# Kernel tuning notes

Hardware: AMD Instinct MI355X
Metric: run time of the kernel (lower is better)

Reference implementation:

```python
import jax, jax.numpy as jnp
import numpy as np

IN_DIM = 3072
OUT_DIM = 3072
NUM_GROUPS = 12
RANK = 1024
IN_PG = IN_DIM // NUM_GROUPS    # 256
OUT_PG = OUT_DIM // NUM_GROUPS  # 256


def _xavier_uniform(key, shape):
    # torch xavier_uniform on a 3D tensor treats dim0*..*dim[-2] as fan_in-ish;
    # torch uses fan_in = shape[-1]*prod(shape[1:-1])? Actually for >2D,
    # fan_in = shape[1] * receptive_field, fan_out = shape[0] * receptive_field.
    # For (g, i, r): fan_in = i * r? torch: fan_in = size(1)*rf, fan_out = size(0)*rf
    # where rf = prod(shape[2:]). So fan_in = shape[1]*shape[2], fan_out = shape[0]*shape[2].
    rf = int(np.prod(shape[2:])) if len(shape) > 2 else 1
    fan_in = shape[1] * rf
    fan_out = shape[0] * rf
    limit = float(np.sqrt(6.0 / (fan_in + fan_out)))
    return jax.random.uniform(key, shape, jnp.float32, -limit, limit)


def setup_inputs() -> dict:
    key = jax.random.key(0)
    kx, kd, ku = jax.random.split(key, 3)
    x = jax.random.normal(kx, (2, 4096, IN_DIM), jnp.float32)
    down = _xavier_uniform(kd, (NUM_GROUPS, IN_PG, RANK))
    up = _xavier_uniform(ku, (NUM_GROUPS, RANK, OUT_PG))
    mix = jnp.zeros((NUM_GROUPS, NUM_GROUPS, RANK), jnp.float32)
    idx = jnp.arange(NUM_GROUPS)
    mix = mix.at[idx, idx, :].set(1.0)
    return {"x": x, "down": down, "mix": mix, "up": up}


def reference(x, down, mix, up):
    b, l, _ = x.shape
    xg = x.reshape(b, l, NUM_GROUPS, IN_PG)          # [b,l,g,i]
    z = jnp.einsum('blgi,gir->blgr', xg, down)       # grouped down-project
    z = jnp.einsum('blgr,ghr->blhr', z, mix)         # per-rank group mix (12x12)
    y = jnp.einsum('blhr,hro->blho', z, up)          # grouped up-project
    return y.reshape(b, l, OUT_DIM)
```

## Files before the change

### kernel.cpp

```cpp
#include <hip/hip_runtime.h>
#include <stdint.h>

typedef short  s16x8 __attribute__((ext_vector_type(8)));
typedef short  s16x4 __attribute__((ext_vector_type(4)));
typedef float  f32x4 __attribute__((ext_vector_type(4)));
typedef unsigned short ushort_t;

#define G_AS __attribute__((address_space(1)))
#define L_AS __attribute__((address_space(3)))

__device__ __forceinline__ void gl_lds16(const void* g, void* l) {
    __builtin_amdgcn_global_load_lds((const G_AS uint32_t*)g, (L_AS uint32_t*)l, 16, 0, 0);
}

__device__ __forceinline__ float b2f(ushort_t u) {
    union { uint32_t i; float f; } v; v.i = ((uint32_t)u) << 16; return v.f;
}
__device__ __forceinline__ ushort_t f2b(float f) {
    uint32_t x = __float_as_uint(f);
    x += 0x7FFF + ((x >> 16) & 1);
    return (ushort_t)(x >> 16);
}

#define MFMA16(a, b, c) __builtin_amdgcn_mfma_f32_16x16x32_bf16((a), (b), (c), 0, 0, 0)

__global__ __launch_bounds__(256) void k_cvt(const float* __restrict__ src,
                                             ushort_t* __restrict__ dst, int n8) {
    int idx = blockIdx.x * 256 + threadIdx.x;
    int stride = gridDim.x * 256;
    for (int i = idx; i < n8; i += stride) {
        f32x4 a = *(const f32x4*)(src + (size_t)i * 8);
        f32x4 b = *(const f32x4*)(src + (size_t)i * 8 + 4);
        s16x8 v;
#pragma unroll
        for (int j = 0; j < 4; ++j) { v[j] = (short)f2b(a[j]); v[j + 4] = (short)f2b(b[j]); }
        *(s16x8*)(dst + (size_t)i * 8) = v;
    }
}

__global__ __launch_bounds__(256) void k_transpose_up(const float* __restrict__ up,
                                                      ushort_t* __restrict__ upT) {
    int bid = blockIdx.x;
    int h  = bid >> 6;
    int rt = (bid >> 2) & 15;
    int ot = bid & 3;
    int r0 = rt << 6, o0 = ot << 6;
    __shared__ ushort_t tile[64][72];
    int t = threadIdx.x;
    const float* src = up + ((size_t)h << 18) + (size_t)r0 * 256 + o0;
#pragma unroll
    for (int p = 0; p < 2; ++p) {
        int rr = (t >> 3) + (p << 5);
        int cc = (t & 7) << 3;
        f32x4 va = *(const f32x4*)(src + rr * 256 + cc);
        f32x4 vb = *(const f32x4*)(src + rr * 256 + cc + 4);
#pragma unroll
        for (int j = 0; j < 4; ++j) {
            tile[rr][cc + j]     = f2b(va[j]);
            tile[rr][cc + 4 + j] = f2b(vb[j]);
        }
    }
    __syncthreads();
    ushort_t* dst = upT + ((size_t)h << 18) + (size_t)o0 * 1024 + r0;
#pragma unroll
    for (int p = 0; p < 2; ++p) {
        int oo = (t >> 3) + (p << 5);
        int rr = (t & 7) << 3;
        s16x8 v;
#pragma unroll
        for (int j = 0; j < 8; ++j) v[j] = (short)tile[rr + j][oo];
        *(s16x8*)(dst + (size_t)oo * 1024 + rr) = v;
    }
}

__global__ __launch_bounds__(256) void k_build_w(const ushort_t* __restrict__ downB,
                                                 const float* __restrict__ mixp,
                                                 const ushort_t* __restrict__ upT,
                                                 ushort_t* __restrict__ WT) {
    int bid = blockIdx.x;
    int gh = bid >> 2;
    int g = gh / 12, h = gh % 12;
    int it = (bid >> 1) & 1, ot = bid & 1;
    int i0 = it << 7, o0 = ot << 7;

    const ushort_t* A    = downB + ((size_t)g << 18);
    const ushort_t* Bt   = upT   + ((size_t)h << 18);
    const float*    mrow = mixp  + (size_t)(g * 12 + h) * 1024;

    __shared__ ushort_t As[128 * 64];
    __shared__ ushort_t Bs[128 * 64];

    int tid  = threadIdx.x;
    int lane = tid & 63, wave = tid >> 6;
    int wr = wave >> 1, wc = wave & 1;
    int lr = lane & 15;
    int kq = (lane >> 4) << 3;

    f32x4 acc[4][4] = {};

    for (int kk = 0; kk < 1024; kk += 64) {
        __syncthreads();
#pragma unroll
        for (int j = 0; j < 4; ++j) {
            int off = (j << 12) + (wave << 10) + (lane << 4);
            int row = off >> 7;
            int kc  = (off & 127) >> 1;
            gl_lds16(A  + (size_t)(i0 + row) * 1024 + kk + kc, (char*)As + off);
            gl_lds16(Bt + (size_t)(o0 + row) * 1024 + kk + kc, (char*)Bs + off);
        }
        __syncthreads();
#pragma unroll
        for (int ks = 0; ks < 64; ks += 32) {
            f32x4 m0 = *(const f32x4*)(mrow + kk + ks + kq);
            f32x4 m1 = *(const f32x4*)(mrow + kk + ks + kq + 4);
            float mf[8];
#pragma unroll
            for (int j = 0; j < 4; ++j) { mf[j] = m0[j]; mf[j + 4] = m1[j]; }

            s16x8 bfr[4];
#pragma unroll
            for (int b = 0; b < 4; ++b) {
                s16x8 raw = *(const s16x8*)&Bs[(wc * 64 + b * 16 + lr) * 64 + ks + kq];
#pragma unroll
                for (int j = 0; j < 8; ++j)
                    bfr[b][j] = (short)f2b(b2f((ushort_t)raw[j]) * mf[j]);
            }
            s16x8 afr[4];
#pragma unroll
            for (int a = 0; a < 4; ++a)
                afr[a] = *(const s16x8*)&As[(wr * 64 + a * 16 + lr) * 64 + ks + kq];
#pragma unroll
            for (int a = 0; a < 4; ++a)
#pragma unroll
                for (int b = 0; b < 4; ++b)
                    acc[a][b] = MFMA16(afr[a], bfr[b], acc[a][b]);
        }
    }

    int colbase = g * 256 + i0 + wr * 64;
    int rowbase = h * 256 + o0 + wc * 64;
#pragma unroll
    for (int a = 0; a < 4; ++a)
#pragma unroll
        for (int b = 0; b < 4; ++b) {
            int o = rowbase + b * 16 + lr;
            int i = colbase + a * 16 + ((lane >> 4) << 2);
            s16x4 pv;
#pragma unroll
            for (int v = 0; v < 4; ++v) pv[v] = (short)f2b(acc[a][b][v]);
            *(s16x4*)(WT + (size_t)o * 3072 + i) = pv;
        }
}

#define BAR() __builtin_amdgcn_s_barrier()
#define WAITV(n) asm volatile("s_waitcnt vmcnt(" #n ")" ::: "memory")
#define WAITL() asm volatile("s_waitcnt lgkmcnt(0)" ::: "memory")

__global__ __launch_bounds__(512, 1) void k_main8(const ushort_t* __restrict__ X,
                                                  const ushort_t* __restrict__ WT,
                                                  float* __restrict__ Y) {
    extern __shared__ ushort_t lds[];
    int bid = blockIdx.x;
    int wg  = (bid & 7) * 48 + (bid >> 3);
    int tt = wg / 12, nt = wg % 12;
    int m0 = tt << 8, n0 = nt << 8;

    int tid  = threadIdx.x;
    int lane = tid & 63;
    int wave = tid >> 6;
    int wr = wave >> 2;
    int wc = wave & 3;
    int lr = lane & 15;
    int cq = lane >> 4;

    auto STAGE = [&](int buf, int op, int kh, int t) {
        const ushort_t* src = op ? WT : X;
        int rb = op ? n0 : m0;
        int kb = t * 64 + kh * 32;
        ushort_t* base = lds + buf * 32768 + op * 16384 + kh * 8192;
#pragma unroll
        for (int j = 0; j < 2; ++j) {
            int boff = (j << 13) + (tid << 4);
            int r  = boff >> 6;
            int ch = (boff >> 4) & 3;
            int ks = kb + ((ch ^ ((r >> 1) & 3)) << 3);
            gl_lds16(src + (size_t)(rb + r) * 3072 + ks, (char*)base + boff);
        }
    };
    auto RD = [&](int buf, int op, int kh, int fr) -> s16x8 {
        int row = (op ? wc * 64 : wr * 128) + fr * 16 + lr;
        int off = buf * 32768 + op * 16384 + kh * 8192 + row * 32
                + ((cq ^ ((row >> 1) & 3)) << 3);
        return *(const s16x8*)(lds + off);
    };

    f32x4 acc[8][4] = {};
    s16x8 af[4], bf[4];

#define PH_READ_AB(mlo, kh) { _Pragma("unroll") for (int i = 0; i < 4; ++i) af[i] = RD(cur, 0, kh, (mlo) + i); \
                              _Pragma("unroll") for (int i = 0; i < 4; ++i) bf[i] = RD(cur, 1, kh, i); }
#define PH_READ_A(mlo, kh)  { _Pragma("unroll") for (int i = 0; i < 4; ++i) af[i] = RD(cur, 0, kh, (mlo) + i); }
#define PH_MFMA(mlo)        { __builtin_amdgcn_s_setprio(1); \
                              _Pragma("unroll") for (int mi = 0; mi < 4; ++mi) \
                              _Pragma("unroll") for (int ni = 0; ni < 4; ++ni) \
                                  acc[(mlo) + mi][ni] = MFMA16(af[mi], bf[ni], acc[(mlo) + mi][ni]); \
                              __builtin_amdgcn_s_setprio(0); }

    STAGE(0, 0, 0, 0); STAGE(0, 1, 0, 0); STAGE(0, 0, 1, 0); STAGE(0, 1, 1, 0);
    WAITV(4); BAR();

    int cur = 0;
    for (int t = 0; t < 47; ++t) {
        int nx = cur ^ 1;
        PH_READ_AB(0, 0); STAGE(nx, 0, 0, t + 1);
        BAR(); WAITL(); PH_MFMA(0); BAR();
        PH_READ_A(4, 0);  STAGE(nx, 1, 0, t + 1);
        BAR(); WAITL(); PH_MFMA(4); WAITV(4); BAR();
        PH_READ_AB(0, 1); STAGE(nx, 0, 1, t + 1);
        BAR(); WAITL(); PH_MFMA(0); BAR();
        PH_READ_A(4, 1);  STAGE(nx, 1, 1, t + 1);
        BAR(); WAITL(); PH_MFMA(4); WAITV(4); BAR();
        cur = nx;
    }
    PH_READ_AB(0, 0); BAR(); WAITL(); PH_MFMA(0); BAR();
    PH_READ_A(4, 0);  BAR(); WAITL(); PH_MFMA(4); WAITV(0); BAR();
    PH_READ_AB(0, 1); BAR(); WAITL(); PH_MFMA(0); BAR();
    PH_READ_A(4, 1);  BAR(); WAITL(); PH_MFMA(4);

    int trow = m0 + wr * 128 + (cq << 2);
    int ncol = n0 + wc * 64 + lr;
#pragma unroll
    for (int mi = 0; mi < 8; ++mi)
#pragma unroll
        for (int ni = 0; ni < 4; ++ni) {
            int rr = trow + mi * 16;
            int cc = ncol + ni * 16;
#pragma unroll
            for (int v = 0; v < 4; ++v)
                Y[(size_t)(rr + v) * 3072 + cc] = acc[mi][ni][v];
        }
}

extern "C" void kernel_launch(void* const* d_in, const int* in_sizes, int n_in,
                              void* d_out, int out_size, void* d_ws, size_t ws_size,
                              hipStream_t stream) {
    const float* x    = (const float*)d_in[0];
    const float* down = (const float*)d_in[1];
    const float* mixp = (const float*)d_in[2];
    const float* up   = (const float*)d_in[3];
    float* out = (float*)d_out;

    ushort_t* WT    = (ushort_t*)d_ws;
    ushort_t* upT   = WT    + (size_t)3072 * 3072;
    ushort_t* downB = upT   + (size_t)12 * 256 * 1024;
    ushort_t* xB    = downB + (size_t)12 * 256 * 1024;

    static int lds_attr_set = 0;
    if (!lds_attr_set) {
        hipFuncSetAttribute((const void*)k_main8,
                            hipFuncAttributeMaxDynamicSharedMemorySize, 131072);
        lds_attr_set = 1;
    }

    k_cvt         <<<dim3(1536), dim3(256), 0, stream>>>(down, downB, 393216);
    k_transpose_up<<<dim3(768),  dim3(256), 0, stream>>>(up, upT);
    k_build_w     <<<dim3(576),  dim3(256), 0, stream>>>(downB, mixp, upT, WT);
    k_cvt         <<<dim3(2048), dim3(256), 0, stream>>>(x, xB, 3145728);
    k_main8       <<<dim3(384),  dim3(512), 131072, stream>>>(xB, WT, out);
}
```

Measured before the change: 410.6 us.

## Merge up-transpose and x conversion kernels, fold down conversion and mix into build_w

Combines the up-transpose and the x fp32-to-bf16 conversion into one launch split by block index, and removes the separate down-conversion kernel. k_build_w now reads fp32 down directly, multiplies it by the mix row, and writes the bf16 product into LDS, so the B operand no longer needs per-fragment unpack, scale and repack. This cuts two kernel launches and a round trip of down through global memory, and moves the mix scaling from B to A. The cost is that the A tile is loaded synchronously through registers instead of with async global-to-LDS loads.

New measurement: 465.6 us. 1.13x slower.

```diff
diff --git a/kernel.cpp b/kernel.cpp
--- a/kernel.cpp
+++ b/kernel.cpp
@@ -24,56 +24,57 @@
 
 #define MFMA16(a, b, c) __builtin_amdgcn_mfma_f32_16x16x32_bf16((a), (b), (c), 0, 0, 0)
 
-__global__ __launch_bounds__(256) void k_cvt(const float* __restrict__ src,
-                                             ushort_t* __restrict__ dst, int n8) {
-    int idx = blockIdx.x * 256 + threadIdx.x;
-    int stride = gridDim.x * 256;
-    for (int i = idx; i < n8; i += stride) {
-        f32x4 a = *(const f32x4*)(src + (size_t)i * 8);
-        f32x4 b = *(const f32x4*)(src + (size_t)i * 8 + 4);
-        s16x8 v;
-#pragma unroll
-        for (int j = 0; j < 4; ++j) { v[j] = (short)f2b(a[j]); v[j + 4] = (short)f2b(b[j]); }
-        *(s16x8*)(dst + (size_t)i * 8) = v;
-    }
-}
-
-__global__ __launch_bounds__(256) void k_transpose_up(const float* __restrict__ up,
-                                                      ushort_t* __restrict__ upT) {
-    int bid = blockIdx.x;
-    int h  = bid >> 6;
-    int rt = (bid >> 2) & 15;
-    int ot = bid & 3;
-    int r0 = rt << 6, o0 = ot << 6;
-    __shared__ ushort_t tile[64][72];
-    int t = threadIdx.x;
-    const float* src = up + ((size_t)h << 18) + (size_t)r0 * 256 + o0;
-#pragma unroll
-    for (int p = 0; p < 2; ++p) {
-        int rr = (t >> 3) + (p << 5);
-        int cc = (t & 7) << 3;
-        f32x4 va = *(const f32x4*)(src + rr * 256 + cc);
-        f32x4 vb = *(const f32x4*)(src + rr * 256 + cc + 4);
-#pragma unroll
-        for (int j = 0; j < 4; ++j) {
-            tile[rr][cc + j]     = f2b(va[j]);
-            tile[rr][cc + 4 + j] = f2b(vb[j]);
-        }
-    }
-    __syncthreads();
-    ushort_t* dst = upT + ((size_t)h << 18) + (size_t)o0 * 1024 + r0;
-#pragma unroll
-    for (int p = 0; p < 2; ++p) {
-        int oo = (t >> 3) + (p << 5);
-        int rr = (t & 7) << 3;
-        s16x8 v;
-#pragma unroll
-        for (int j = 0; j < 8; ++j) v[j] = (short)tile[rr + j][oo];
-        *(s16x8*)(dst + (size_t)oo * 1024 + rr) = v;
-    }
-}
-
-__global__ __launch_bounds__(256) void k_build_w(const ushort_t* __restrict__ downB,
+__global__ __launch_bounds__(256) void k_prep(const float* __restrict__ up,
+                                              ushort_t* __restrict__ upT,
+                                              const float* __restrict__ x,
+                                              ushort_t* __restrict__ xB) {
+    int b = blockIdx.x;
+    if (b < 768) {
+        int h  = b >> 6;
+        int rt = (b >> 2) & 15;
+        int ot = b & 3;
+        int r0 = rt << 6, o0 = ot << 6;
+        __shared__ ushort_t tile[64][72];
+        int t = threadIdx.x;
+        const float* src = up + ((size_t)h << 18) + (size_t)r0 * 256 + o0;
+#pragma unroll
+        for (int p = 0; p < 2; ++p) {
+            int rr = (t >> 3) + (p << 5);
+            int cc = (t & 7) << 3;
+            f32x4 va = *(const f32x4*)(src + rr * 256 + cc);
+            f32x4 vb = *(const f32x4*)(src + rr * 256 + cc + 4);
+#pragma unroll
+            for (int j = 0; j < 4; ++j) {
+                tile[rr][cc + j]     = f2b(va[j]);
+                tile[rr][cc + 4 + j] = f2b(vb[j]);
+            }
+        }
+        __syncthreads();
+        ushort_t* dst = upT + ((size_t)h << 18) + (size_t)o0 * 1024 + r0;
+#pragma unroll
+        for (int p = 0; p < 2; ++p) {
+            int oo = (t >> 3) + (p << 5);
+            int rr = (t & 7) << 3;
+            s16x8 v;
+#pragma unroll
+            for (int j = 0; j < 8; ++j) v[j] = (short)tile[rr + j][oo];
+            *(s16x8*)(dst + (size_t)oo * 1024 + rr) = v;
+        }
+    } else {
+        int idx = (b - 768) * 256 + threadIdx.x;
+        int stride = 2048 * 256;
+        for (int i = idx; i < 3145728; i += stride) {
+            f32x4 a = *(const f32x4*)(x + (size_t)i * 8);
+            f32x4 c = *(const f32x4*)(x + (size_t)i * 8 + 4);
+            s16x8 v;
+#pragma unroll
+            for (int j = 0; j < 4; ++j) { v[j] = (short)f2b(a[j]); v[j + 4] = (short)f2b(c[j]); }
+            *(s16x8*)(xB + (size_t)i * 8) = v;
+        }
+    }
+}
+
+__global__ __launch_bounds__(256) void k_build_w(const float* __restrict__ down,
                                                  const float* __restrict__ mixp,
                                                  const ushort_t* __restrict__ upT,
                                                  ushort_t* __restrict__ WT) {
@@ -83,9 +84,8 @@
     int it = (bid >> 1) & 1, ot = bid & 1;
     int i0 = it << 7, o0 = ot << 7;
 
-    const ushort_t* A    = downB + ((size_t)g << 18);
-    const ushort_t* Bt   = upT   + ((size_t)h << 18);
-    const float*    mrow = mixp  + (size_t)(g * 12 + h) * 1024;
+    const ushort_t* Bt   = upT + ((size_t)h << 18);
+    const float*    mrow = mixp + (size_t)gh * 1024;
 
     __shared__ ushort_t As[128 * 64];
     __shared__ ushort_t Bs[128 * 64];
@@ -96,39 +96,51 @@
     int lr = lane & 15;
     int kq = (lane >> 4) << 3;
 
+    int arow = tid >> 1;
+    int akh  = (tid & 1) << 5;
+    const float* asrc = down + ((size_t)g << 18) + (size_t)(i0 + arow) * 1024 + akh;
+    const float* msrc = mrow + akh;
+    ushort_t*    adst = As + arow * 64 + akh;
+
     f32x4 acc[4][4] = {};
 
     for (int kk = 0; kk < 1024; kk += 64) {
         __syncthreads();
 #pragma unroll
         for (int j = 0; j < 4; ++j) {
-            int off = (j << 12) + (wave << 10) + (lane << 4);
+            int off = (j << 12) + (tid << 4);
             int row = off >> 7;
             int kc  = (off & 127) >> 1;
-            gl_lds16(A  + (size_t)(i0 + row) * 1024 + kk + kc, (char*)As + off);
             gl_lds16(Bt + (size_t)(o0 + row) * 1024 + kk + kc, (char*)Bs + off);
         }
+        {
+            f32x4 d[8], mm[8];
+#pragma unroll
+            for (int j = 0; j < 8; ++j) {
+                d[j]  = *(const f32x4*)(asrc + kk + j * 4);
+                mm[j] = *(const f32x4*)(msrc + kk + j * 4);
+            }
+#pragma unroll
+            for (int j = 0; j < 4; ++j) {
+                s16x8 w;
+#pragma unroll
+                for (int v = 0; v < 4; ++v) {
+                    w[v]     = (short)f2b(d[2 * j][v]     * mm[2 * j][v]);
+                    w[v + 4] = (short)f2b(d[2 * j + 1][v] * mm[2 * j + 1][v]);
+                }
+                *(s16x8*)(adst + j * 8) = w;
+            }
+        }
         __syncthreads();
 #pragma unroll
         for (int ks = 0; ks < 64; ks += 32) {
-            f32x4 m0 = *(const f32x4*)(mrow + kk + ks + kq);
-            f32x4 m1 = *(const f32x4*)(mrow + kk + ks + kq + 4);
-            float mf[8];
-#pragma unroll
-            for (int j = 0; j < 4; ++j) { mf[j] = m0[j]; mf[j + 4] = m1[j]; }
-
-            s16x8 bfr[4];
-#pragma unroll
-            for (int b = 0; b < 4; ++b) {
-                s16x8 raw = *(const s16x8*)&Bs[(wc * 64 + b * 16 + lr) * 64 + ks + kq];
-#pragma unroll
-                for (int j = 0; j < 8; ++j)
-                    bfr[b][j] = (short)f2b(b2f((ushort_t)raw[j]) * mf[j]);
-            }
-            s16x8 afr[4];
+            s16x8 afr[4], bfr[4];
 #pragma unroll
             for (int a = 0; a < 4; ++a)
                 afr[a] = *(const s16x8*)&As[(wr * 64 + a * 16 + lr) * 64 + ks + kq];
+#pragma unroll
+            for (int b = 0; b < 4; ++b)
+                bfr[b] = *(const s16x8*)&Bs[(wc * 64 + b * 16 + lr) * 64 + ks + kq];
 #pragma unroll
             for (int a = 0; a < 4; ++a)
 #pragma unroll
@@ -250,10 +262,9 @@
     const float* up   = (const float*)d_in[3];
     float* out = (float*)d_out;
 
-    ushort_t* WT    = (ushort_t*)d_ws;
-    ushort_t* upT   = WT    + (size_t)3072 * 3072;
-    ushort_t* downB = upT   + (size_t)12 * 256 * 1024;
-    ushort_t* xB    = downB + (size_t)12 * 256 * 1024;
+    ushort_t* WT  = (ushort_t*)d_ws;
+    ushort_t* upT = WT  + (size_t)3072 * 3072;
+    ushort_t* xB  = upT + (size_t)12 * 256 * 1024;
 
     static int lds_attr_set = 0;
     if (!lds_attr_set) {
@@ -262,9 +273,7 @@
         lds_attr_set = 1;
     }
 
-    k_cvt         <<<dim3(1536), dim3(256), 0, stream>>>(down, downB, 393216);
-    k_transpose_up<<<dim3(768),  dim3(256), 0, stream>>>(up, upT);
-    k_build_w     <<<dim3(576),  dim3(256), 0, stream>>>(downB, mixp, upT, WT);
-    k_cvt         <<<dim3(2048), dim3(256), 0, stream>>>(x, xB, 3145728);
-    k_main8       <<<dim3(384),  dim3(512), 131072, stream>>>(xB, WT, out);
-}
+    k_prep   <<<dim3(2816), dim3(256), 0, stream>>>(up, upT, x, xB);
+    k_build_w<<<dim3(576),  dim3(256), 0, stream>>>(down, mixp, upT, WT);
+    k_main8  <<<dim3(384),  dim3(512), 131072, stream>>>(xB, WT, out);
+}
```
